# Kernel tuning notes

Measured on AMD Instinct MI355X. Metric: run time of the kernel, lower is better.

The kernel has to match this reference:

```python
import jax, jax.numpy as jnp
import numpy as np
from jax import lax

DIM = 64
K = 3
GROUPS = 1
NUM_KERNELS = 4
B, H, W = 32, 128, 128


def setup_inputs() -> dict:
    key = jax.random.key(0)
    k1, k2, k3, k4 = jax.random.split(key, 4)
    x = jax.random.normal(k1, (B, DIM, H, W), dtype=jnp.float32)
    attention = jax.random.uniform(k2, (B, NUM_KERNELS), dtype=jnp.float32)
    # kaiming-uniform-like init per kernel: bound = sqrt(6 / fan_in)
    fan_in = (DIM // GROUPS) * K * K
    bound = float(np.sqrt(6.0 / fan_in))
    weight = jax.random.uniform(k3, (NUM_KERNELS, DIM, DIM // GROUPS, K, K),
                                dtype=jnp.float32, minval=-bound, maxval=bound)
    bias_p = jax.random.normal(k4, (NUM_KERNELS, DIM), dtype=jnp.float32) * 0.1
    return {"x": x, "attention": attention, "weight": weight, "bias_p": bias_p}


def reference(x, attention, weight, bias_p):
    # Mix kernel bank per sample: [B, nk] @ [nk, dim*dim//g*k*k]
    w_flat = weight.reshape(NUM_KERNELS, -1)
    w_mix = (attention @ w_flat).reshape(B, DIM, DIM // GROUPS, K, K)
    b_mix = attention @ bias_p  # [B, dim]

    def conv_one(xb, wb, bb):
        # xb: [C,H,W], wb: [C_out, C_in//g, k, k]
        out = lax.conv_general_dilated(
            xb[None], wb, window_strides=(1, 1), padding="SAME",
            dimension_numbers=("NCHW", "OIHW", "NCHW"),
            feature_group_count=GROUPS)
        return out[0] + bb[:, None, None]

    return jax.vmap(conv_one)(x, w_mix, b_mix)  # [B, dim, H, W]
```

## Files before the change

### kernel.cpp

```cpp
#include <hip/hip_runtime.h>


#define DIM 64
#define BATCH 32
#define HH 128
#define WW 128
#define NK 4

typedef __attribute__((ext_vector_type(4))) float f32x4;
typedef __attribute__((ext_vector_type(8))) short bf16x8;
typedef __attribute__((ext_vector_type(8))) unsigned short ushort8;

static __device__ __forceinline__ unsigned short f2bf(float f) {
    union { float f; unsigned u; } v; v.f = f;
    unsigned r = v.u + 0x7fffu + ((v.u >> 16) & 1u);
    return (unsigned short)(r >> 16);
}

__global__ __launch_bounds__(256) void mix_weights(
    const float* __restrict__ w, const float* __restrict__ att,
    unsigned short* __restrict__ wmix) {
    __shared__ float tr[4][576];
    int wave = threadIdx.x >> 6, lane = threadIdx.x & 63;
    int idx = blockIdx.x * 4 + wave;
    int b = idx >> 6, co = idx & 63;
    float a[NK];
    #pragma unroll
    for (int k = 0; k < NK; ++k) a[k] = att[b * NK + k];
    float s[9];
    #pragma unroll
    for (int t = 0; t < 9; ++t) s[t] = 0.f;
    #pragma unroll
    for (int k = 0; k < NK; ++k) {
        const float* wp = w + (size_t)(k * DIM + co) * 576;
        #pragma unroll
        for (int t = 0; t < 9; ++t)
            s[t] += a[k] * wp[t * 64 + lane];
    }
    #pragma unroll
    for (int t = 0; t < 9; ++t) tr[wave][t * 64 + lane] = s[t];
    __syncthreads();
    #pragma unroll
    for (int t = 0; t < 9; ++t) {
        float v = tr[wave][lane * 9 + t];
        wmix[(((size_t)b * 9 + t) * DIM + co) * DIM + lane] = f2bf(v);
    }
}

__global__ __launch_bounds__(256) void mix_bias(
    const float* __restrict__ bias, const float* __restrict__ att,
    float* __restrict__ bmix) {
    int idx = blockIdx.x * 256 + threadIdx.x;
    if (idx >= BATCH * DIM) return;
    int b = idx >> 6, co = idx & 63;
    float s = 0.f;
    for (int k = 0; k < NK; ++k) s += att[b * NK + k] * bias[k * DIM + co];
    bmix[idx] = s;
}

__global__ __launch_bounds__(256, 2) void conv_mfma(
    const float* __restrict__ x, const unsigned short* __restrict__ wmix,
    const float* __restrict__ bmix, float* __restrict__ out) {

    __shared__ unsigned short Xs[6 * 66 * 64];
    __shared__ unsigned short Ws[2][64 * 64];

    int bid = blockIdx.x;
    int b   = bid >> 6;
    int r6  = bid & 63;
    int h0  = (r6 >> 1) * 4;
    int w0  = (r6 & 1) * 64;

    int tid  = threadIdx.x;
    int wave = tid >> 6, lane = tid & 63;
    int l15  = lane & 15, q = lane >> 4;

    const int ch0 = tid, ch1 = tid + 256;
    const int co0 = ch0 >> 3, gp0 = ch0 & 7;
    const int co1 = ch1 >> 3, gp1 = ch1 & 7;
    const unsigned short* wsA = wmix + (size_t)b * 9 * 4096 + co0 * 64 + ((gp0 ^ (co0 & 7)) << 3);
    const unsigned short* wsB = wmix + (size_t)b * 9 * 4096 + co1 * 64 + ((gp1 ^ (co1 & 7)) << 3);
    ushort8 wr0 = *(const ushort8*)(wsA);
    ushort8 wr1 = *(const ushort8*)(wsB);

    float biasr[4][4];
    #pragma unroll
    for (int mt = 0; mt < 4; ++mt)
        #pragma unroll
        for (int rg = 0; rg < 4; ++rg)
            biasr[mt][rg] = bmix[b * DIM + mt * 16 + q * 4 + rg];

    #pragma unroll
    for (int half = 0; half < 2; ++half) {
        f32x4 xv[3][4];
        #pragma unroll
        for (int rr = 0; rr < 3; ++rr) {
            int r = half * 3 + rr;
            int hin = h0 - 1 + r;
            bool ok = (hin >= 0) && (hin < HH);
            #pragma unroll
            for (int it = 0; it < 4; ++it) {
                int lin = it * 256 + tid;
                int ci = lin >> 4, c4 = lin & 15;
                f32x4 v = {0.f, 0.f, 0.f, 0.f};
                if (ok)
                    v = *(const f32x4*)&x[(((size_t)b * DIM + ci) * HH + hin) * WW + w0 + c4 * 4];
                xv[rr][it] = v;
            }
        }
        #pragma unroll
        for (int rr = 0; rr < 3; ++rr) {
            int r = half * 3 + rr;
            #pragma unroll
            for (int it = 0; it < 4; ++it) {
                int lin = it * 256 + tid;
                int ci = lin >> 4, c4 = lin & 15;
                #pragma unroll
                for (int j = 0; j < 4; ++j) {
                    int c = c4 * 4 + 1 + j;
                    Xs[(r * 66 + c) * 64 + (((ci >> 3) ^ ((c >> 1) & 7)) << 3) + (ci & 7)] =
                        f2bf(xv[rr][it][j]);
                }
            }
        }
    }
    #pragma unroll
    for (int e = 0; e < 3; ++e) {
        int item = e * 256 + tid;
        int edge = item >= 384;
        int jj = item - edge * 384;
        int ci = jj & 63, r = jj >> 6;
        int hin = h0 - 1 + r;
        int win = edge ? (w0 + 64) : (w0 - 1);
        float v = 0.f;
        if (hin >= 0 && hin < HH && win >= 0 && win < WW)
            v = x[(((size_t)b * DIM + ci) * HH + hin) * WW + win];
        int c = edge ? 65 : 0;
        Xs[(r * 66 + c) * 64 + (((ci >> 3) ^ ((c >> 1) & 7)) << 3) + (ci & 7)] = f2bf(v);
    }

    *(ushort8*)&Ws[0][co0 * 64 + gp0 * 8] = wr0;
    *(ushort8*)&Ws[0][co1 * 64 + gp1 * 8] = wr1;
    wr0 = *(const ushort8*)(wsA + 4096);
    wr1 = *(const ushort8*)(wsB + 4096);

    f32x4 acc[4][4];
    f32x4 zero = {0.f, 0.f, 0.f, 0.f};
    #pragma unroll
    for (int mt = 0; mt < 4; ++mt)
        #pragma unroll
        for (int nt = 0; nt < 4; ++nt) acc[mt][nt] = zero;

    __syncthreads();

    #pragma unroll
    for (int tap = 0; tap < 9; ++tap) {
        int buf = tap & 1;
        if (tap < 8) {
            *(ushort8*)&Ws[buf ^ 1][co0 * 64 + gp0 * 8] = wr0;
            *(ushort8*)&Ws[buf ^ 1][co1 * 64 + gp1 * 8] = wr1;
            if (tap < 7) {
                wr0 = *(const ushort8*)(wsA + (tap + 2) * 4096);
                wr1 = *(const ushort8*)(wsB + (tap + 2) * 4096);
            }
        }
        int kh = tap / 3, kw = tap - kh * 3;
        int r = wave + kh;
        #pragma unroll
        for (int s = 0; s < 2; ++s) {
            int g = s * 4 + q;
            bf16x8 af[4], bfr[4];
            #pragma unroll
            for (int mt = 0; mt < 4; ++mt) {
                int co = mt * 16 + l15;
                af[mt] = *(const bf16x8*)&Ws[buf][co * 64 + ((g ^ (co & 7)) << 3)];
            }
            #pragma unroll
            for (int nt = 0; nt < 4; ++nt) {
                int c = nt * 16 + l15 + kw;
                bfr[nt] = *(const bf16x8*)&Xs[(r * 66 + c) * 64 + ((g ^ ((c >> 1) & 7)) << 3)];
            }
            #pragma unroll
            for (int mt = 0; mt < 4; ++mt)
                #pragma unroll
                for (int nt = 0; nt < 4; ++nt)
                    acc[mt][nt] = __builtin_amdgcn_mfma_f32_16x16x32_bf16(
                        af[mt], bfr[nt], acc[mt][nt], 0, 0, 0);
        }
        __syncthreads();
    }

    int h = h0 + wave;
    #pragma unroll
    for (int mt = 0; mt < 4; ++mt) {
        #pragma unroll
        for (int nt = 0; nt < 4; ++nt) {
            int wcol = w0 + nt * 16 + l15;
            #pragma unroll
            for (int rg = 0; rg < 4; ++rg) {
                int co = mt * 16 + q * 4 + rg;
                out[(((size_t)b * DIM + co) * HH + h) * WW + wcol] = acc[mt][nt][rg] + biasr[mt][rg];
            }
        }
    }
}

extern "C" void kernel_launch(void* const* d_in, const int* in_sizes, int n_in,
                              void* d_out, int out_size, void* d_ws, size_t ws_size,
                              hipStream_t stream) {
    const float* x   = (const float*)d_in[0];
    const float* att = (const float*)d_in[1];
    const float* wgt = (const float*)d_in[2];
    const float* bia = (const float*)d_in[3];
    float* out = (float*)d_out;

    unsigned short* wmix = (unsigned short*)d_ws;
    float* bmix = (float*)((char*)d_ws + 2359296);

    mix_weights<<<512, 256, 0, stream>>>(wgt, att, wmix);
    mix_bias<<<8, 256, 0, stream>>>(bia, att, bmix);
    conv_mfma<<<2048, 256, 0, stream>>>(x, wmix, bmix, out);
}
```

Baseline: 262.1 us.

## Load pre-swizzled MFMA weight fragments directly from global, drop LDS weight staging

The weight-mix kernel now writes mixed weights in the exact per-lane MFMA A-fragment order, so the conv kernel loads A fragments straight from global/L2 into registers with one-step prefetch. This removes the double-buffered LDS weight tile and the per-tap barriers. The x staging also packs two channels per 32-bit LDS store, and block indices are remapped across XCDs. Occupancy is raised to 3 blocks per CU, and the bias load moves to the epilogue. The risk is more global load latency on the MFMA critical path and higher register pressure under the new launch bound.

```diff
diff --git a/kernel.cpp b/kernel.cpp
--- a/kernel.cpp
+++ b/kernel.cpp
@@ -15,6 +15,9 @@
     union { float f; unsigned u; } v; v.f = f;
     unsigned r = v.u + 0x7fffu + ((v.u >> 16) & 1u);
     return (unsigned short)(r >> 16);
+}
+static __device__ __forceinline__ unsigned pack2(float a, float b) {
+    return (unsigned)f2bf(a) | ((unsigned)f2bf(b) << 16);
 }
 
 __global__ __launch_bounds__(256) void mix_weights(
@@ -40,10 +43,14 @@
     #pragma unroll
     for (int t = 0; t < 9; ++t) tr[wave][t * 64 + lane] = s[t];
     __syncthreads();
+    int mt = co >> 4;
+    int lo = ((lane >> 3) & 3) * 16 + (co & 15);
+    int ss = lane >> 5;
+    int jj = lane & 7;
     #pragma unroll
     for (int t = 0; t < 9; ++t) {
         float v = tr[wave][lane * 9 + t];
-        wmix[(((size_t)b * 9 + t) * DIM + co) * DIM + lane] = f2bf(v);
+        wmix[(size_t)((((b * 9 + t) * 2 + ss) * 4 + mt) * 64 + lo) * 8 + jj] = f2bf(v);
     }
 }
 
@@ -58,14 +65,14 @@
     bmix[idx] = s;
 }
 
-__global__ __launch_bounds__(256, 2) void conv_mfma(
+__global__ __launch_bounds__(256, 3) void conv_mfma(
     const float* __restrict__ x, const unsigned short* __restrict__ wmix,
     const float* __restrict__ bmix, float* __restrict__ out) {
 
     __shared__ unsigned short Xs[6 * 66 * 64];
-    __shared__ unsigned short Ws[2][64 * 64];
 
     int bid = blockIdx.x;
+    bid = (bid & 7) * 256 + (bid >> 3);
     int b   = bid >> 6;
     int r6  = bid & 63;
     int h0  = (r6 >> 1) * 4;
@@ -75,51 +82,35 @@
     int wave = tid >> 6, lane = tid & 63;
     int l15  = lane & 15, q = lane >> 4;
 
-    const int ch0 = tid, ch1 = tid + 256;
-    const int co0 = ch0 >> 3, gp0 = ch0 & 7;
-    const int co1 = ch1 >> 3, gp1 = ch1 & 7;
-    const unsigned short* wsA = wmix + (size_t)b * 9 * 4096 + co0 * 64 + ((gp0 ^ (co0 & 7)) << 3);
-    const unsigned short* wsB = wmix + (size_t)b * 9 * 4096 + co1 * 64 + ((gp1 ^ (co1 & 7)) << 3);
-    ushort8 wr0 = *(const ushort8*)(wsA);
-    ushort8 wr1 = *(const ushort8*)(wsB);
-
-    float biasr[4][4];
-    #pragma unroll
-    for (int mt = 0; mt < 4; ++mt)
-        #pragma unroll
-        for (int rg = 0; rg < 4; ++rg)
-            biasr[mt][rg] = bmix[b * DIM + mt * 16 + q * 4 + rg];
-
     #pragma unroll
     for (int half = 0; half < 2; ++half) {
-        f32x4 xv[3][4];
+        f32x4 xv[3][2][2];
         #pragma unroll
         for (int rr = 0; rr < 3; ++rr) {
             int r = half * 3 + rr;
             int hin = h0 - 1 + r;
             bool ok = (hin >= 0) && (hin < HH);
             #pragma unroll
-            for (int it = 0; it < 4; ++it) {
-                int lin = it * 256 + tid;
-                int ci = lin >> 4, c4 = lin & 15;
-                f32x4 v = {0.f, 0.f, 0.f, 0.f};
-                if (ok)
-                    v = *(const f32x4*)&x[(((size_t)b * DIM + ci) * HH + hin) * WW + w0 + c4 * 4];
-                xv[rr][it] = v;
+            for (int it = 0; it < 2; ++it) {
+                int slot = it * 256 + tid;
+                int p = slot >> 4, c4 = slot & 15;
+                f32x4 z = {0.f, 0.f, 0.f, 0.f};
+                xv[rr][it][0] = ok ? *(const f32x4*)&x[(((size_t)b * DIM + 2 * p    ) * HH + hin) * WW + w0 + c4 * 4] : z;
+                xv[rr][it][1] = ok ? *(const f32x4*)&x[(((size_t)b * DIM + 2 * p + 1) * HH + hin) * WW + w0 + c4 * 4] : z;
             }
         }
         #pragma unroll
         for (int rr = 0; rr < 3; ++rr) {
             int r = half * 3 + rr;
             #pragma unroll
-            for (int it = 0; it < 4; ++it) {
-                int lin = it * 256 + tid;
-                int ci = lin >> 4, c4 = lin & 15;
+            for (int it = 0; it < 2; ++it) {
+                int slot = it * 256 + tid;
+                int p = slot >> 4, c4 = slot & 15;
                 #pragma unroll
                 for (int j = 0; j < 4; ++j) {
                     int c = c4 * 4 + 1 + j;
-                    Xs[(r * 66 + c) * 64 + (((ci >> 3) ^ ((c >> 1) & 7)) << 3) + (ci & 7)] =
-                        f2bf(xv[rr][it][j]);
+                    int xi = (r * 66 + c) * 64 + (((p >> 2) ^ ((c >> 1) & 7)) << 3) + 2 * (p & 3);
+                    *(unsigned*)&Xs[xi] = pack2(xv[rr][it][0][j], xv[rr][it][1][j]);
                 }
             }
         }
@@ -139,10 +130,11 @@
         Xs[(r * 66 + c) * 64 + (((ci >> 3) ^ ((c >> 1) & 7)) << 3) + (ci & 7)] = f2bf(v);
     }
 
-    *(ushort8*)&Ws[0][co0 * 64 + gp0 * 8] = wr0;
-    *(ushort8*)&Ws[0][co1 * 64 + gp1 * 8] = wr1;
-    wr0 = *(const ushort8*)(wsA + 4096);
-    wr1 = *(const ushort8*)(wsB + 4096);
+    const unsigned short* wa = wmix + (size_t)b * 9 * 4096;
+    bf16x8 afp[4];
+    #pragma unroll
+    for (int mt = 0; mt < 4; ++mt)
+        afp[mt] = *(const bf16x8*)&wa[(size_t)(mt * 64 + lane) * 8];
 
     f32x4 acc[4][4];
     f32x4 zero = {0.f, 0.f, 0.f, 0.f};
@@ -155,26 +147,21 @@
 
     #pragma unroll
     for (int tap = 0; tap < 9; ++tap) {
-        int buf = tap & 1;
-        if (tap < 8) {
-            *(ushort8*)&Ws[buf ^ 1][co0 * 64 + gp0 * 8] = wr0;
-            *(ushort8*)&Ws[buf ^ 1][co1 * 64 + gp1 * 8] = wr1;
-            if (tap < 7) {
-                wr0 = *(const ushort8*)(wsA + (tap + 2) * 4096);
-                wr1 = *(const ushort8*)(wsB + (tap + 2) * 4096);
-            }
-        }
         int kh = tap / 3, kw = tap - kh * 3;
         int r = wave + kh;
         #pragma unroll
         for (int s = 0; s < 2; ++s) {
+            int u = tap * 2 + s;
+            bf16x8 afc[4];
+            #pragma unroll
+            for (int mt = 0; mt < 4; ++mt) afc[mt] = afp[mt];
+            if (u < 17) {
+                #pragma unroll
+                for (int mt = 0; mt < 4; ++mt)
+                    afp[mt] = *(const bf16x8*)&wa[(size_t)(((u + 1) * 4 + mt) * 64 + lane) * 8];
+            }
             int g = s * 4 + q;
-            bf16x8 af[4], bfr[4];
-            #pragma unroll
-            for (int mt = 0; mt < 4; ++mt) {
-                int co = mt * 16 + l15;
-                af[mt] = *(const bf16x8*)&Ws[buf][co * 64 + ((g ^ (co & 7)) << 3)];
-            }
+            bf16x8 bfr[4];
             #pragma unroll
             for (int nt = 0; nt < 4; ++nt) {
                 int c = nt * 16 + l15 + kw;
@@ -185,11 +172,16 @@
                 #pragma unroll
                 for (int nt = 0; nt < 4; ++nt)
                     acc[mt][nt] = __builtin_amdgcn_mfma_f32_16x16x32_bf16(
-                        af[mt], bfr[nt], acc[mt][nt], 0, 0, 0);
-        }
-        __syncthreads();
-    }
-
+                        afc[mt], bfr[nt], acc[mt][nt], 0, 0, 0);
+        }
+    }
+
+    float biasr[4][4];
+    #pragma unroll
+    for (int mt = 0; mt < 4; ++mt)
+        #pragma unroll
+        for (int rg = 0; rg < 4; ++rg)
+            biasr[mt][rg] = bmix[b * DIM + mt * 16 + q * 4 + rg];
     int h = h0 + wave;
     #pragma unroll
     for (int mt = 0; mt < 4; ++mt) {
```

New measurement: 268.8 us. +2.5%, slower.
